# Kernel optimization log

Measured on AMD Instinct MI355X. Metric: run time of the kernel, lower is better.

Reference implementation:

```python
import jax, jax.numpy as jnp
import numpy as np

N = 4096  # size of every layer (I, H1, H2, O)
EPS = 1e-5  # torch LayerNorm default


def _ln(x, g, b):
    # torch.nn.LayerNorm: biased variance, affine
    mu = jnp.mean(x)
    xc = x - mu
    v = jnp.mean(xc * xc)
    return xc * jax.lax.rsqrt(v + EPS) * g + b


def setup_inputs() -> dict:
    key = jax.random.key(0)
    ks = jax.random.split(key, 24)
    W = 0.02  # weight scale ~ uniform-init magnitude of nn.Linear at fan_in=4096
    inp = {
        "input_raw": jax.random.normal(ks[0], (N,), jnp.float32),
        "h1_prev": jax.random.normal(ks[1], (N,), jnp.float32),
        "h2_prev": jax.random.normal(ks[2], (N,), jnp.float32),
        "W_I_H1": jax.random.normal(ks[3], (N, N), jnp.float32) * W,
        "W_H1_H1": jax.random.normal(ks[4], (N, N), jnp.float32) * W,
        "W_H1_H2": jax.random.normal(ks[5], (N, N), jnp.float32) * W,
        "W_H2_H1": jax.random.normal(ks[6], (N, N), jnp.float32) * W,
        "W_H2_H2": jax.random.normal(ks[7], (N, N), jnp.float32) * W,
        "W_H1_O": jax.random.normal(ks[8], (N, N), jnp.float32) * W,
        "W_H2_O": jax.random.normal(ks[9], (N, N), jnp.float32) * W,
        "bias_h1": jax.random.normal(ks[10], (N,), jnp.float32) * 0.1,
        "bias_h2": jax.random.normal(ks[11], (N,), jnp.float32) * 0.1,
        "bias_o": jax.random.normal(ks[12], (N,), jnp.float32) * 0.1,
        "g_i": jax.random.uniform(ks[13], (N,), jnp.float32, 0.5, 1.5),
        "b_i": jax.random.normal(ks[14], (N,), jnp.float32) * 0.1,
        "g_h1": jax.random.uniform(ks[15], (N,), jnp.float32, 0.5, 1.5),
        "bln_h1": jax.random.normal(ks[16], (N,), jnp.float32) * 0.1,
        "g_h2": jax.random.uniform(ks[17], (N,), jnp.float32, 0.5, 1.5),
        "bln_h2": jax.random.normal(ks[18], (N,), jnp.float32) * 0.1,
        "g_o": jax.random.uniform(ks[19], (N,), jnp.float32, 0.5, 1.5),
        "bln_o": jax.random.normal(ks[20], (N,), jnp.float32) * 0.1,
    }
    return inp


def reference(input_raw, h1_prev, h2_prev,
              W_I_H1, W_H1_H1, W_H1_H2, W_H2_H1, W_H2_H2, W_H1_O, W_H2_O,
              bias_h1, bias_h2, bias_o,
              g_i, b_i, g_h1, bln_h1, g_h2, bln_h2, g_o, bln_o):
    # --- Phase 1: feedback accumulation + per-layer LayerNorm ---
    # I and O have no feedback -> LN(zeros) = LN bias (beta)
    i_out = b_i + input_raw                       # layers['I']: LN(0) then += input_raw
    h1_fb = _ln(W_H1_H1 @ h1_prev, g_h1, bln_h1)  # self-recurrent feedback H1->H1
    h2_fb = _ln(W_H2_H2 @ h2_prev, g_h2, bln_h2)  # self-recurrent feedback H2->H2
    o_init = bln_o                                # layers['O']: LN(zeros)

    # --- Phase 2: input-driven / feedback-only hidden activations ---
    h1_p2 = jax.nn.relu(_ln(W_I_H1 @ i_out + h1_fb + bias_h1, g_h1, bln_h1))  # 'I' in forward
    h2_p2 = jax.nn.relu(_ln(h2_fb + bias_h2, g_h2, bln_h2))                    # feedback-only

    # --- Phase 3: inter-hidden forward pass (intermediate_output OVERWRITES) ---
    h1_f = jax.nn.relu(_ln(W_H2_H1 @ h2_p2 + bias_h1, g_h1, bln_h1))
    h2_f = jax.nn.relu(_ln(W_H1_H2 @ h1_p2 + bias_h2, g_h2, bln_h2))

    # --- Output layer: sum forwards, tanh(LN(.)) ---
    o = jnp.tanh(_ln(o_init + W_H1_O @ h1_f + W_H2_O @ h2_f + bias_o, g_o, bln_o))
    return o
```

## Files before the change

kernel.cpp:

```cpp
#include <hip/hip_runtime.h>
#include <math.h>

#define NN 4096
#define NV4 1024


__device__ __forceinline__ float4 ld4(const float* __restrict__ p, int t) {
    return reinterpret_cast<const float4*>(p)[t];
}
__device__ __forceinline__ void st4(float* __restrict__ p, int t, float4 v) {
    reinterpret_cast<float4*>(p)[t] = v;
}
__device__ __forceinline__ float4 add4(float4 a, float4 b) {
    return make_float4(a.x + b.x, a.y + b.y, a.z + b.z, a.w + b.w);
}

__device__ __forceinline__ float2 block_reduce2(float s, float ss, float* sbuf) {
    #pragma unroll
    for (int off = 32; off > 0; off >>= 1) {
        s  += __shfl_down(s,  off, 64);
        ss += __shfl_down(ss, off, 64);
    }
    const int wave = threadIdx.x >> 6;
    const int lane = threadIdx.x & 63;
    if (lane == 0) { sbuf[wave] = s; sbuf[16 + wave] = ss; }
    __syncthreads();
    float rs = 0.f, rss = 0.f;
    if (threadIdx.x < 16) { rs = sbuf[threadIdx.x]; rss = sbuf[16 + threadIdx.x]; }
    if (wave == 0) {
        #pragma unroll
        for (int off = 8; off > 0; off >>= 1) {
            rs  += __shfl_down(rs,  off, 64);
            rss += __shfl_down(rss, off, 64);
        }
        if (lane == 0) { sbuf[0] = rs; sbuf[1] = rss; }
    }
    __syncthreads();
    float2 r = make_float2(sbuf[0], sbuf[1]);
    __syncthreads();
    return r;
}

struct LNStat { float mu, rstd; };

__device__ __forceinline__ LNStat ln_stats(float4 v, float* sbuf) {
    float s  = v.x + v.y + v.z + v.w;
    float ss = v.x * v.x + v.y * v.y + v.z * v.z + v.w * v.w;
    float2 r = block_reduce2(s, ss, sbuf);
    LNStat o;
    o.mu = r.x * (1.0f / NN);
    float var = r.y * (1.0f / NN) - o.mu * o.mu;
    o.rstd = rsqrtf(var + 1e-5f);
    return o;
}

__device__ __forceinline__ float4 ln_apply(float4 v, LNStat st, float4 g, float4 b) {
    return make_float4((v.x - st.mu) * st.rstd * g.x + b.x,
                       (v.y - st.mu) * st.rstd * g.y + b.y,
                       (v.z - st.mu) * st.rstd * g.z + b.z,
                       (v.w - st.mu) * st.rstd * g.w + b.w);
}

__device__ __forceinline__ float4 relu4(float4 v) {
    return make_float4(fmaxf(v.x, 0.f), fmaxf(v.y, 0.f), fmaxf(v.z, 0.f), fmaxf(v.w, 0.f));
}


__device__ __forceinline__ void gemv_row(const float* __restrict__ W,
                                         const float* __restrict__ x,
                                         float* __restrict__ y,
                                         const float* __restrict__ xadd) {
    const int wave = threadIdx.x >> 6;
    const int lane = threadIdx.x & 63;
    const int row  = (blockIdx.x << 2) + wave;
    const float4* __restrict__ Wr = reinterpret_cast<const float4*>(W + (size_t)row * NN);
    const float4* __restrict__ x4 = reinterpret_cast<const float4*>(x);
    float acc = 0.f;
    #pragma unroll
    for (int it = 0; it < 16; ++it) {
        const int j = (it << 6) + lane;
        float4 w  = Wr[j];
        float4 xv = x4[j];
        if (xadd) {
            float4 a = reinterpret_cast<const float4*>(xadd)[j];
            xv = add4(xv, a);
        }
        acc = fmaf(w.x, xv.x, acc);
        acc = fmaf(w.y, xv.y, acc);
        acc = fmaf(w.z, xv.z, acc);
        acc = fmaf(w.w, xv.w, acc);
    }
    #pragma unroll
    for (int off = 32; off > 0; off >>= 1) acc += __shfl_down(acc, off, 64);
    if (lane == 0) y[row] = acc;
}

__global__ __launch_bounds__(256) void gemv_stageA(
    const float* __restrict__ W_H1_H1, const float* __restrict__ h1_prev,
    const float* __restrict__ W_H2_H2, const float* __restrict__ h2_prev,
    const float* __restrict__ W_I_H1,  const float* __restrict__ input_raw,
    const float* __restrict__ b_i,
    float* __restrict__ mv1, float* __restrict__ mv2, float* __restrict__ mv3)
{
    if (blockIdx.y == 0)      gemv_row(W_H1_H1, h1_prev,   mv1, nullptr);
    else if (blockIdx.y == 1) gemv_row(W_H2_H2, h2_prev,   mv2, nullptr);
    else                      gemv_row(W_I_H1,  input_raw, mv3, b_i);
}

__global__ __launch_bounds__(256) void gemv_pair(
    const float* __restrict__ Wa, const float* __restrict__ xa, float* __restrict__ ya,
    const float* __restrict__ Wb, const float* __restrict__ xb, float* __restrict__ yb)
{
    if (blockIdx.y == 0) gemv_row(Wa, xa, ya, nullptr);
    else                 gemv_row(Wb, xb, yb, nullptr);
}

__global__ __launch_bounds__(1024) void phase2_kernel(
    const float* __restrict__ mv1, const float* __restrict__ mv2, const float* __restrict__ mv3,
    const float* __restrict__ bias_h1, const float* __restrict__ bias_h2,
    const float* __restrict__ g_h1, const float* __restrict__ bln_h1,
    const float* __restrict__ g_h2, const float* __restrict__ bln_h2,
    float* __restrict__ h1_p2, float* __restrict__ h2_p2)
{
    __shared__ float sbuf[32];
    const int t = threadIdx.x;
    if (blockIdx.x == 0) {
        float4 g = ld4(g_h1, t), b = ld4(bln_h1, t);
        float4 v = ld4(mv1, t);
        LNStat s1 = ln_stats(v, sbuf);
        float4 fb = ln_apply(v, s1, g, b);
        float4 tt = add4(add4(ld4(mv3, t), fb), ld4(bias_h1, t));
        LNStat s2 = ln_stats(tt, sbuf);
        st4(h1_p2, t, relu4(ln_apply(tt, s2, g, b)));
    } else {
        float4 g = ld4(g_h2, t), b = ld4(bln_h2, t);
        float4 v = ld4(mv2, t);
        LNStat s1 = ln_stats(v, sbuf);
        float4 fb = ln_apply(v, s1, g, b);
        float4 tt = add4(fb, ld4(bias_h2, t));
        LNStat s2 = ln_stats(tt, sbuf);
        st4(h2_p2, t, relu4(ln_apply(tt, s2, g, b)));
    }
}

__global__ __launch_bounds__(1024) void phase3_kernel(
    const float* __restrict__ mv4, const float* __restrict__ mv5,
    const float* __restrict__ bias_h1, const float* __restrict__ bias_h2,
    const float* __restrict__ g_h1, const float* __restrict__ bln_h1,
    const float* __restrict__ g_h2, const float* __restrict__ bln_h2,
    float* __restrict__ h1_f, float* __restrict__ h2_f)
{
    __shared__ float sbuf[32];
    const int t = threadIdx.x;
    const float* mv;  const float* bias; const float* g; const float* b; float* out;
    if (blockIdx.x == 0) { mv = mv4; bias = bias_h1; g = g_h1; b = bln_h1; out = h1_f; }
    else                 { mv = mv5; bias = bias_h2; g = g_h2; b = bln_h2; out = h2_f; }
    float4 v = add4(ld4(mv, t), ld4(bias, t));
    LNStat s = ln_stats(v, sbuf);
    st4(out, t, relu4(ln_apply(v, s, ld4(g, t), ld4(b, t))));
}

__global__ __launch_bounds__(1024) void final_kernel(
    const float* __restrict__ mv6, const float* __restrict__ mv7,
    const float* __restrict__ bias_o, const float* __restrict__ bln_o,
    const float* __restrict__ g_o,
    float* __restrict__ out)
{
    __shared__ float sbuf[32];
    const int t = threadIdx.x;
    float4 v = add4(add4(ld4(bln_o, t), ld4(mv6, t)), add4(ld4(mv7, t), ld4(bias_o, t)));
    LNStat s = ln_stats(v, sbuf);
    float4 r = ln_apply(v, s, ld4(g_o, t), ld4(bln_o, t));
    st4(out, t, make_float4(tanhf(r.x), tanhf(r.y), tanhf(r.z), tanhf(r.w)));
}


extern "C" void kernel_launch(void* const* d_in, const int* in_sizes, int n_in,
                              void* d_out, int out_size, void* d_ws, size_t ws_size,
                              hipStream_t stream) {
    const float* input_raw = (const float*)d_in[0];
    const float* h1_prev   = (const float*)d_in[1];
    const float* h2_prev   = (const float*)d_in[2];
    const float* W_I_H1    = (const float*)d_in[3];
    const float* W_H1_H1   = (const float*)d_in[4];
    const float* W_H1_H2   = (const float*)d_in[5];
    const float* W_H2_H1   = (const float*)d_in[6];
    const float* W_H2_H2   = (const float*)d_in[7];
    const float* W_H1_O    = (const float*)d_in[8];
    const float* W_H2_O    = (const float*)d_in[9];
    const float* bias_h1   = (const float*)d_in[10];
    const float* bias_h2   = (const float*)d_in[11];
    const float* bias_o    = (const float*)d_in[12];
    const float* b_i       = (const float*)d_in[14];
    const float* g_h1      = (const float*)d_in[15];
    const float* bln_h1    = (const float*)d_in[16];
    const float* g_h2      = (const float*)d_in[17];
    const float* bln_h2    = (const float*)d_in[18];
    const float* g_o       = (const float*)d_in[19];
    const float* bln_o     = (const float*)d_in[20];

    float* ws    = (float*)d_ws;
    float* mv1   = ws;
    float* mv2   = ws + 1 * NN;
    float* mv3   = ws + 2 * NN;
    float* h1_p2 = ws + 3 * NN;
    float* h2_p2 = ws + 4 * NN;
    float* mv4   = ws + 5 * NN;
    float* mv5   = ws + 6 * NN;
    float* h1_f  = ws + 7 * NN;
    float* h2_f  = ws + 8 * NN;
    float* mv6   = ws + 9 * NN;
    float* mv7   = ws + 10 * NN;

    gemv_stageA<<<dim3(NN / 4, 3), 256, 0, stream>>>(
        W_H1_H1, h1_prev, W_H2_H2, h2_prev, W_I_H1, input_raw, b_i, mv1, mv2, mv3);

    phase2_kernel<<<2, 1024, 0, stream>>>(
        mv1, mv2, mv3, bias_h1, bias_h2, g_h1, bln_h1, g_h2, bln_h2, h1_p2, h2_p2);

    gemv_pair<<<dim3(NN / 4, 2), 256, 0, stream>>>(
        W_H2_H1, h2_p2, mv4, W_H1_H2, h1_p2, mv5);

    phase3_kernel<<<2, 1024, 0, stream>>>(
        mv4, mv5, bias_h1, bias_h2, g_h1, bln_h1, g_h2, bln_h2, h1_f, h2_f);

    gemv_pair<<<dim3(NN / 4, 2), 256, 0, stream>>>(
        W_H1_O, h1_f, mv6, W_H2_O, h2_f, mv7);

    final_kernel<<<1, 1024, 0, stream>>>(
        mv6, mv7, bias_o, bln_o, g_o, (float*)d_out);
}
```

Before: 103.6 us.

## Replace row-per-wave GEMV with grid-strided split-K using atomic accumulation

Reworks all GEMV kernels to stride over the flattened weight matrix with a fixed grid of 512 blocks per matrix. Each wave reduces a 256-element segment and atomically adds it into the output row, which requires zeroing the workspace with a memset first. The first-stage matrices are loaded with nontemporal hints. The aim is better load streaming and fewer blocks, traded against many global atomics, per-iteration shuffle reductions and nondeterministic summation order.

Measured after the change: 139.1 us. 1.34x slower.

```diff
diff --git a/kernel.cpp b/kernel.cpp
--- a/kernel.cpp
+++ b/kernel.cpp
@@ -2,7 +2,11 @@
 #include <math.h>
 
 #define NN 4096
-#define NV4 1024
+#define BLK 256
+#define SKB 512
+#define NITER (NN * NN / 4 / (SKB * BLK))
+
+typedef float f32x4 __attribute__((ext_vector_type(4)));
 
 
 __device__ __forceinline__ float4 ld4(const float* __restrict__ p, int t) {
@@ -66,53 +70,54 @@
 }
 
 
-__device__ __forceinline__ void gemv_row(const float* __restrict__ W,
-                                         const float* __restrict__ x,
-                                         float* __restrict__ y,
-                                         const float* __restrict__ xadd) {
-    const int wave = threadIdx.x >> 6;
+template<int NT>
+__device__ __forceinline__ void splitk_core(const float* __restrict__ W,
+                                            const float* __restrict__ x,
+                                            const float* __restrict__ xa,
+                                            float* __restrict__ y) {
+    const f32x4*  W4 = reinterpret_cast<const f32x4*>(W);
+    const float4* x4 = reinterpret_cast<const float4*>(x);
+    const float4* a4 = reinterpret_cast<const float4*>(xa);
     const int lane = threadIdx.x & 63;
-    const int row  = (blockIdx.x << 2) + wave;
-    const float4* __restrict__ Wr = reinterpret_cast<const float4*>(W + (size_t)row * NN);
-    const float4* __restrict__ x4 = reinterpret_cast<const float4*>(x);
-    float acc = 0.f;
-    #pragma unroll
-    for (int it = 0; it < 16; ++it) {
-        const int j = (it << 6) + lane;
-        float4 w  = Wr[j];
-        float4 xv = x4[j];
-        if (xadd) {
-            float4 a = reinterpret_cast<const float4*>(xadd)[j];
-            xv = add4(xv, a);
-        }
-        acc = fmaf(w.x, xv.x, acc);
-        acc = fmaf(w.y, xv.y, acc);
-        acc = fmaf(w.z, xv.z, acc);
-        acc = fmaf(w.w, xv.w, acc);
-    }
-    #pragma unroll
-    for (int off = 32; off > 0; off >>= 1) acc += __shfl_down(acc, off, 64);
-    if (lane == 0) y[row] = acc;
-}
-
-__global__ __launch_bounds__(256) void gemv_stageA(
+    const int base = blockIdx.x * BLK + threadIdx.x;
+    #pragma unroll 4
+    for (int s = 0; s < NITER; ++s) {
+        const int i = base + s * (SKB * BLK);
+        f32x4 w;
+        if (NT) w = __builtin_nontemporal_load(W4 + i);
+        else    w = W4[i];
+        const int c = i & (NN / 4 - 1);
+        float4 xv = x4[c];
+        if (xa) xv = add4(xv, a4[c]);
+        float p = fmaf(w.x, xv.x, fmaf(w.y, xv.y, fmaf(w.z, xv.z, w.w * xv.w)));
+        #pragma unroll
+        for (int off = 32; off > 0; off >>= 1) p += __shfl_down(p, off, 64);
+        if (lane == 0) atomicAdd(y + (i >> 10), p);
+    }
+}
+
+__global__ __launch_bounds__(BLK) void gemv_stageA(
     const float* __restrict__ W_H1_H1, const float* __restrict__ h1_prev,
     const float* __restrict__ W_H2_H2, const float* __restrict__ h2_prev,
     const float* __restrict__ W_I_H1,  const float* __restrict__ input_raw,
     const float* __restrict__ b_i,
     float* __restrict__ mv1, float* __restrict__ mv2, float* __restrict__ mv3)
 {
-    if (blockIdx.y == 0)      gemv_row(W_H1_H1, h1_prev,   mv1, nullptr);
-    else if (blockIdx.y == 1) gemv_row(W_H2_H2, h2_prev,   mv2, nullptr);
-    else                      gemv_row(W_I_H1,  input_raw, mv3, b_i);
-}
-
-__global__ __launch_bounds__(256) void gemv_pair(
-    const float* __restrict__ Wa, const float* __restrict__ xa, float* __restrict__ ya,
-    const float* __restrict__ Wb, const float* __restrict__ xb, float* __restrict__ yb)
-{
-    if (blockIdx.y == 0) gemv_row(Wa, xa, ya, nullptr);
-    else                 gemv_row(Wb, xb, yb, nullptr);
+    const float* W; const float* x; const float* xa; float* y;
+    if (blockIdx.y == 0)      { W = W_H1_H1; x = h1_prev;   xa = nullptr; y = mv1; }
+    else if (blockIdx.y == 1) { W = W_H2_H2; x = h2_prev;   xa = nullptr; y = mv2; }
+    else                      { W = W_I_H1;  x = input_raw; xa = b_i;     y = mv3; }
+    splitk_core<1>(W, x, xa, y);
+}
+
+__global__ __launch_bounds__(BLK) void gemv_pair(
+    const float* __restrict__ Wa, const float* __restrict__ xva, float* __restrict__ ya,
+    const float* __restrict__ Wb, const float* __restrict__ xvb, float* __restrict__ yb)
+{
+    const float* W; const float* x; float* y;
+    if (blockIdx.y == 0) { W = Wa; x = xva; y = ya; }
+    else                 { W = Wb; x = xvb; y = yb; }
+    splitk_core<0>(W, x, nullptr, y);
 }
 
 __global__ __launch_bounds__(1024) void phase2_kernel(
@@ -212,19 +217,21 @@
     float* mv6   = ws + 9 * NN;
     float* mv7   = ws + 10 * NN;
 
-    gemv_stageA<<<dim3(NN / 4, 3), 256, 0, stream>>>(
+    hipMemsetAsync(ws, 0, 11 * NN * sizeof(float), stream);
+
+    gemv_stageA<<<dim3(SKB, 3), BLK, 0, stream>>>(
         W_H1_H1, h1_prev, W_H2_H2, h2_prev, W_I_H1, input_raw, b_i, mv1, mv2, mv3);
 
     phase2_kernel<<<2, 1024, 0, stream>>>(
         mv1, mv2, mv3, bias_h1, bias_h2, g_h1, bln_h1, g_h2, bln_h2, h1_p2, h2_p2);
 
-    gemv_pair<<<dim3(NN / 4, 2), 256, 0, stream>>>(
+    gemv_pair<<<dim3(SKB, 2), BLK, 0, stream>>>(
         W_H2_H1, h2_p2, mv4, W_H1_H2, h1_p2, mv5);
 
     phase3_kernel<<<2, 1024, 0, stream>>>(
         mv4, mv5, bias_h1, bias_h2, g_h1, bln_h1, g_h2, bln_h2, h1_f, h2_f);
 
-    gemv_pair<<<dim3(NN / 4, 2), 256, 0, stream>>>(
+    gemv_pair<<<dim3(SKB, 2), BLK, 0, stream>>>(
         W_H1_O, h1_f, mv6, W_H2_O, h2_f, mv7);
 
     final_kernel<<<1, 1024, 0, stream>>>(
```
